# Performance work log

Measured on AMD Instinct MI355X. Metric: run time of the kernel, lower is better.

The kernel has to match this reference:

```python
import jax, jax.numpy as jnp
import numpy as np

AB = 8            # activation quant bits
NOISE_LEVEL = 0.1
CY_SCALE = 2.0    # stands in for args.cy_scale
B, IN, H = 8192, 512, 512


def _fake_quant(x, bits, sign):
    # forward: clip/clamp then round-to-grid; backward (STE) handled elsewhere
    if sign:
        delta = 1.0 / (2.0 ** (bits - 1))
        xc = jnp.clip(x, -1.0 + delta, 1.0 - delta)
        scale = 2.0 ** (bits - 1)
    else:
        xc = jnp.clip(x, 0.0, 1.0)
        scale = 2.0 ** bits
    q = jnp.round(xc * scale) / scale
    # STE: identity gradient w.r.t. x
    return x + jax.lax.stop_gradient(q - x)


def setup_inputs() -> dict:
    key = jax.random.key(0)
    ks = jax.random.split(key, 11)
    return {
        "input": jax.random.normal(ks[0], (B, IN), jnp.float32),
        "hx": jax.random.normal(ks[1], (B, H), jnp.float32),
        "cx": jax.random.normal(ks[2], (B, H), jnp.float32),
        "weight_ih": jax.random.normal(ks[3], (4 * H, IN), jnp.float32),
        "weight_hh": jax.random.normal(ks[4], (4 * H, H), jnp.float32),
        "bias_ih": jax.random.normal(ks[5], (4 * H,), jnp.float32),
        "bias_hh": jax.random.normal(ks[6], (4 * H,), jnp.float32),
        "noise_ih": jax.random.normal(ks[7], (IN, 4 * H), jnp.float32),
        "noise_hh": jax.random.normal(ks[8], (H, 4 * H), jnp.float32),
        "noise_bias_ih": jax.random.normal(ks[9], (4 * H,), jnp.float32),
        "noise_bias_hh": jax.random.normal(ks[10], (4 * H,), jnp.float32),
    }


def reference(input, hx, cx, weight_ih, weight_hh, bias_ih, bias_hh,
              noise_ih, noise_hh, noise_bias_ih, noise_bias_hh):
    # noisy weights: noise = randn * w.max() * noise_level (raw randn passed in)
    w_ih = weight_ih.T + noise_ih * (jnp.max(weight_ih) * NOISE_LEVEL)   # [IN,4H]
    w_hh = weight_hh.T + noise_hh * (jnp.max(weight_hh) * NOISE_LEVEL)   # [H,4H]
    b_ih = bias_ih + noise_bias_ih * (jnp.max(bias_ih) * NOISE_LEVEL)
    b_hh = bias_hh + noise_bias_hh * (jnp.max(bias_hh) * NOISE_LEVEL)

    gates = input @ w_ih + b_ih + hx @ w_hh + b_hh                        # [B,4H]
    ingate, forgetgate, cellgate, outgate = jnp.split(gates, 4, axis=1)

    ingate = _fake_quant(jax.nn.sigmoid(ingate), AB, False)
    forgetgate = _fake_quant(jax.nn.sigmoid(forgetgate), AB, False)
    cellgate = _fake_quant(jnp.tanh(cellgate), AB, True)
    outgate = _fake_quant(jax.nn.sigmoid(outgate), AB, False)

    cy = _fake_quant(
        (_fake_quant(forgetgate * cx, AB, True)
         + _fake_quant(ingate * cellgate, AB, True)) / CY_SCALE,
        AB, True)
    hy = _fake_quant(
        outgate * _fake_quant(jnp.tanh(cy * CY_SCALE), AB, True),
        AB, True)
    return (hy, cy)
```

## Files before the change

### kernel.cpp

```cpp
#include <hip/hip_runtime.h>
#include <cstdint>

typedef unsigned short u16;
typedef __bf16 bf16x8 __attribute__((ext_vector_type(8)));
typedef float f32x4 __attribute__((ext_vector_type(4)));

#define NB 8192
#define HD 512
#define KD 1024
#define ND 2048
#define HY_OFF (NB * HD)
#define NT 32

__device__ __forceinline__ u16 f2bf(float f) {
  unsigned u = __float_as_uint(f);
  u += 0x7FFFu + ((u >> 16) & 1u);
  return (u16)(u >> 16);
}
__device__ __forceinline__ float bf2f(u16 h) {
  return __uint_as_float(((unsigned)h) << 16);
}
__device__ __forceinline__ void atomicMaxF(float* a, float v) {
  if (v >= 0.f) atomicMax((int*)a, __float_as_int(v));
  else          atomicMin((unsigned int*)a, __float_as_uint(v));
}
__device__ __forceinline__ float fq_u(float x) {
  float xc = fminf(fmaxf(x, 0.0f), 1.0f);
  return rintf(xc * 256.0f) * (1.0f / 256.0f);
}
__device__ __forceinline__ float fq_s(float x) {
  const float lim = 1.0f - 1.0f / 128.0f;
  float xc = fminf(fmaxf(x, -lim), lim);
  return rintf(xc * 128.0f) * (1.0f / 128.0f);
}
__device__ __forceinline__ float sigm(float x) { return 1.0f / (1.0f + expf(-x)); }

__device__ __forceinline__ void gload_lds16(const u16* g, u16* l) {
  __builtin_amdgcn_global_load_lds(
      (const __attribute__((address_space(1))) void*)g,
      (__attribute__((address_space(3))) void*)l, 16, 0, 0);
}

__global__ __launch_bounds__(256) void k_prep_max(
    const float* __restrict__ w_ih, const float* __restrict__ w_hh,
    const float* __restrict__ b_ih, const float* __restrict__ b_hh,
    float* __restrict__ maxes) {
  int bid = blockIdx.x;
  const float* src; int slot, base;
  if (bid < 1024)      { src = w_ih; slot = 0; base = bid * 1024; }
  else if (bid < 2048) { src = w_hh; slot = 1; base = (bid - 1024) * 1024; }
  else if (bid < 2050) { src = b_ih; slot = 2; base = (bid - 2048) * 1024; }
  else                 { src = b_hh; slot = 3; base = (bid - 2050) * 1024; }
  float m = -INFINITY;
  for (int i = threadIdx.x; i < 1024; i += 256) m = fmaxf(m, src[base + i]);
  for (int k = 1; k < 64; k <<= 1) m = fmaxf(m, __shfl_xor(m, k, 64));
  __shared__ float sm[4];
  if ((threadIdx.x & 63) == 0) sm[threadIdx.x >> 6] = m;
  __syncthreads();
  if (threadIdx.x == 0) {
    m = fmaxf(fmaxf(sm[0], sm[1]), fmaxf(sm[2], sm[3]));
    atomicMaxF(&maxes[slot], m);
  }
}

__global__ __launch_bounds__(256) void k_prep_build(
    const float* __restrict__ input, const float* __restrict__ hx,
    const float* __restrict__ w_ih, const float* __restrict__ w_hh,
    const float* __restrict__ n_ih, const float* __restrict__ n_hh,
    const float* __restrict__ b_ih, const float* __restrict__ b_hh,
    const float* __restrict__ nb_ih, const float* __restrict__ nb_hh,
    const float* __restrict__ maxes,
    u16* __restrict__ Xhi, u16* __restrict__ Xlo,
    u16* __restrict__ Whi, u16* __restrict__ Wlo,
    float* __restrict__ biasC) {
  const int bid = blockIdx.x;
  if (bid < 2048) {
    const int total4 = NB * KD / 4;
    for (int e4 = bid * 256 + threadIdx.x; e4 < total4; e4 += 2048 * 256) {
      int row = e4 >> 8;
      int c4  = e4 & 255;
      float4 v = (c4 < 128)
          ? reinterpret_cast<const float4*>(input)[row * 128 + c4]
          : reinterpret_cast<const float4*>(hx)[row * 128 + (c4 - 128)];
      float xs[4] = {v.x, v.y, v.z, v.w};
      ushort4 hi, lo;
      u16 h0 = f2bf(xs[0]); u16 l0 = f2bf(xs[0] - bf2f(h0));
      u16 h1 = f2bf(xs[1]); u16 l1 = f2bf(xs[1] - bf2f(h1));
      u16 h2 = f2bf(xs[2]); u16 l2 = f2bf(xs[2] - bf2f(h2));
      u16 h3 = f2bf(xs[3]); u16 l3 = f2bf(xs[3] - bf2f(h3));
      hi.x = h0; hi.y = h1; hi.z = h2; hi.w = h3;
      lo.x = l0; lo.y = l1; lo.z = l2; lo.w = l3;
      reinterpret_cast<ushort4*>(Xhi)[e4] = hi;
      reinterpret_cast<ushort4*>(Xlo)[e4] = lo;
    }
  } else if (bid < 2176) {
    __shared__ float nT[1024][17];
    const int w  = bid - 2048;
    const int j0 = w * 16;
    const int g  = ((j0 >> 7) & 1) * 2 + ((j0 >> 4) & 1);
    const int hb = ((j0 >> 8) << 2) | ((j0 >> 5) & 3);
    const int col0 = g * 512 + (hb << 4);
    {
      const int cl = threadIdx.x & 15;
      const int kr = threadIdx.x >> 4;
#pragma unroll 4
      for (int i = 0; i < 64; ++i) {
        const int k = kr + 16 * i;
        nT[k][cl] = (k < 512) ? n_ih[k * ND + col0 + cl]
                              : n_hh[(k - 512) * ND + col0 + cl];
      }
    }
    __syncthreads();
    const float s_ih = maxes[0] * 0.1f, s_hh = maxes[1] * 0.1f;
    const int c  = threadIdx.x >> 4;
    const int kl = threadIdx.x & 15;
    const int colL = col0 + c;
    const int j = j0 + c;
#pragma unroll 4
    for (int kk = 0; kk < 16; ++kk) {
      const int k = kk * 64 + kl * 4;
      float4 wv; float s;
      if (k < 512) {
        wv = reinterpret_cast<const float4*>(w_ih)[(colL * 512 + k) >> 2];
        s = s_ih;
      } else {
        wv = reinterpret_cast<const float4*>(w_hh)[(colL * 512 + k - 512) >> 2];
        s = s_hh;
      }
      float xs[4] = {wv.x + nT[k + 0][c] * s, wv.y + nT[k + 1][c] * s,
                     wv.z + nT[k + 2][c] * s, wv.w + nT[k + 3][c] * s};
      ushort4 hi, lo;
      u16 h0 = f2bf(xs[0]); u16 l0 = f2bf(xs[0] - bf2f(h0));
      u16 h1 = f2bf(xs[1]); u16 l1 = f2bf(xs[1] - bf2f(h1));
      u16 h2 = f2bf(xs[2]); u16 l2 = f2bf(xs[2] - bf2f(h2));
      u16 h3 = f2bf(xs[3]); u16 l3 = f2bf(xs[3] - bf2f(h3));
      hi.x = h0; hi.y = h1; hi.z = h2; hi.w = h3;
      lo.x = l0; lo.y = l1; lo.z = l2; lo.w = l3;
      reinterpret_cast<ushort4*>(Whi)[(j * KD + k) >> 2] = hi;
      reinterpret_cast<ushort4*>(Wlo)[(j * KD + k) >> 2] = lo;
    }
  } else {
    int j = (bid - 2176) * 256 + threadIdx.x;
    if (j < ND) {
      int g  = ((j >> 7) & 1) * 2 + ((j >> 4) & 1);
      int hb = ((j >> 8) << 2) | ((j >> 5) & 3);
      int col = g * 512 + (hb << 4) + (j & 15);
      biasC[j] = b_ih[col] + nb_ih[col] * (maxes[2] * 0.1f)
               + b_hh[col] + nb_hh[col] * (maxes[3] * 0.1f);
    }
  }
}

__global__ __launch_bounds__(512, 2) void k_gemm_lstm(
    const u16* __restrict__ Xhi, const u16* __restrict__ Xlo,
    const u16* __restrict__ Whi, const u16* __restrict__ Wlo,
    const float* __restrict__ biasC, const float* __restrict__ cx,
    float* __restrict__ out) {
  __shared__ u16 L[2][4][8192];
  const int tid  = threadIdx.x;
  const int lane = tid & 63, wid = tid >> 6;
  const int wr = wid >> 2, wc = wid & 3;
  const int lr = lane & 15, lg = lane >> 4;
  const int xcd = blockIdx.x & 7, tt = blockIdx.x >> 3;
  const int bm = ((xcd >> 1) << 3) | (tt & 7);
  const int bn = ((xcd & 1) << 2) | (tt >> 3);
  const int mbase = bm * 256, nbase = bn * 256;

  const int l8 = lane >> 3, l7 = lane & 7;
  const int csrc  = l7 ^ l8;
  const int srow  = wid * 16 + 2 * l8 + (csrc >> 2);
  const int skoff = (csrc & 3) * 8;
  const int sdst  = wid * 512;

  const int fro = (lr >> 1) * 64 + ((((lr & 1) << 2) | lg) ^ ((lr >> 1) & 7)) * 8;

  f32x4 acc[8][4] = {};
  bf16x8 afr[4][2];
  bf16x8 bfr[2][2][2];

#define STAGE(V, BUF, HALF)                                                   \
  {                                                                           \
    const u16* arr_ = (BUF) == 0 ? Xhi : (BUF) == 1 ? Xlo                     \
                      : (BUF) == 2 ? Whi : Wlo;                               \
    const int gb_ = ((BUF) < 2 ? mbase : nbase) + (HALF) * 128 + srow;        \
    gload_lds16(arr_ + (size_t)gb_ * KD + (V) * 32 + skoff,                   \
                &L[(V) & 1][(BUF)][(HALF) * 4096 + sdst]);                    \
  }

#define PH2(MH, STAGE_CODE, WAIT_CODE)                                       \
  {                                                                          \
    _Pragma("unroll") for (int m2 = 0; m2 < 4; ++m2) {                       \
      const int ab = ((MH) * 128 + wr * 64 + m2 * 16) * 32 + fro;            \
      afr[m2][0] = *reinterpret_cast<const bf16x8*>(&L[s][0][ab]);           \
      afr[m2][1] = *reinterpret_cast<const bf16x8*>(&L[s][1][ab]);           \
    }                                                                        \
    if ((MH) == 0) {                                                         \
      _Pragma("unroll") for (int nh = 0; nh < 2; ++nh)                       \
        _Pragma("unroll") for (int n2 = 0; n2 < 2; ++n2) {                   \
          const int bb = (nh * 128 + wc * 32 + n2 * 16) * 32 + fro;          \
          bfr[nh][n2][0] = *reinterpret_cast<const bf16x8*>(&L[s][2][bb]);   \
          bfr[nh][n2][1] = *reinterpret_cast<const bf16x8*>(&L[s][3][bb]);   \
        }                                                                    \
    }                                                                        \
    STAGE_CODE;                                                              \
    WAIT_CODE;                                                               \
    __builtin_amdgcn_s_barrier();                                            \
    __builtin_amdgcn_s_setprio(1);                                           \
    _Pragma("unroll") for (int t = 0; t < 3; ++t)                            \
      _Pragma("unroll") for (int m2 = 0; m2 < 4; ++m2)                       \
        _Pragma("unroll") for (int nh = 0; nh < 2; ++nh)                     \
          _Pragma("unroll") for (int n2 = 0; n2 < 2; ++n2) {                 \
            f32x4* ac = &acc[(MH) * 4 + m2][nh * 2 + n2];                    \
            *ac = __builtin_amdgcn_mfma_f32_16x16x32_bf16(                   \
                afr[m2][t == 1], bfr[nh][n2][t == 2], *ac, 0, 0, 0);         \
          }                                                                  \
    __builtin_amdgcn_s_setprio(0);                                           \
    __builtin_amdgcn_s_barrier();                                            \
  }

  STAGE(0, 0, 0); STAGE(0, 1, 0);
  STAGE(0, 2, 0); STAGE(0, 2, 1);
  STAGE(0, 3, 0); STAGE(0, 3, 1);
  STAGE(0, 0, 1); STAGE(0, 1, 1);
  asm volatile("s_waitcnt vmcnt(2)" ::: "memory");
  __builtin_amdgcn_s_barrier();

  int s = 0;
  for (int u = 0; u < NT - 1; ++u, s ^= 1) {
    PH2(0,
        { STAGE(u + 1, 0, 0); STAGE(u + 1, 1, 0);
          STAGE(u + 1, 2, 0); STAGE(u + 1, 2, 1);
          STAGE(u + 1, 3, 0); STAGE(u + 1, 3, 1); },
        asm volatile("s_waitcnt vmcnt(6)" ::: "memory"));
    PH2(1,
        { STAGE(u + 1, 0, 1); STAGE(u + 1, 1, 1); },
        asm volatile("s_waitcnt vmcnt(2)" ::: "memory"));
  }
  PH2(0, , asm volatile("s_waitcnt vmcnt(0)" ::: "memory"));
  PH2(1, , );

#undef PH2
#undef STAGE

  const int hb = bn * 4 + wc;
  const int h = hb * 16 + lr;
  float bias[4];
#pragma unroll
  for (int g = 0; g < 4; ++g)
    bias[g] = biasC[bn * 256 + ((g >> 1) * 8 + wc * 2 + (g & 1)) * 16 + lr];
#pragma unroll
  for (int mh = 0; mh < 2; ++mh) {
#pragma unroll
    for (int m2 = 0; m2 < 4; ++m2) {
      const int m = mh * 4 + m2;
#pragma unroll
      for (int r = 0; r < 4; ++r) {
        const int row = mbase + mh * 128 + wr * 64 + m2 * 16 + lg * 4 + r;
        const float gi = acc[m][0][r] + bias[0];
        const float gf = acc[m][1][r] + bias[1];
        const float gc = acc[m][2][r] + bias[2];
        const float go = acc[m][3][r] + bias[3];
        const float ig = fq_u(sigm(gi));
        const float fg = fq_u(sigm(gf));
        const float cg = fq_s(tanhf(gc));
        const float og = fq_u(sigm(go));
        const float cxv = cx[(size_t)row * HD + h];
        const float t1 = fq_s(fg * cxv);
        const float t2 = fq_s(ig * cg);
        const float cyv = fq_s((t1 + t2) * 0.5f);
        const float hyv = fq_s(og * fq_s(tanhf(cyv * 2.0f)));
        out[(size_t)row * HD + h] = hyv;
        out[HY_OFF + (size_t)row * HD + h] = cyv;
      }
    }
  }
}

extern "C" void kernel_launch(void* const* d_in, const int* in_sizes, int n_in,
                              void* d_out, int out_size, void* d_ws, size_t ws_size,
                              hipStream_t stream) {
  const float* input = (const float*)d_in[0];
  const float* hx    = (const float*)d_in[1];
  const float* cx    = (const float*)d_in[2];
  const float* w_ih  = (const float*)d_in[3];
  const float* w_hh  = (const float*)d_in[4];
  const float* b_ih  = (const float*)d_in[5];
  const float* b_hh  = (const float*)d_in[6];
  const float* n_ih  = (const float*)d_in[7];
  const float* n_hh  = (const float*)d_in[8];
  const float* nb_ih = (const float*)d_in[9];
  const float* nb_hh = (const float*)d_in[10];
  float* out = (float*)d_out;

  char* ws = (char*)d_ws;
  float* maxes = (float*)ws;
  u16* Xhi = (u16*)(ws + 256);
  u16* Xlo = (u16*)(ws + 256 + 16777216);
  u16* Whi = (u16*)(ws + 256 + 2 * 16777216);
  u16* Wlo = (u16*)(ws + 256 + 2 * 16777216 + 4194304);
  float* biasC = (float*)(ws + 256 + 2 * 16777216 + 2 * 4194304);

  hipMemsetAsync(maxes, 0xFF, 16, stream);
  hipLaunchKernelGGL(k_prep_max, dim3(2052), dim3(256), 0, stream,
                     w_ih, w_hh, b_ih, b_hh, maxes);
  hipLaunchKernelGGL(k_prep_build, dim3(2184), dim3(256), 0, stream,
                     input, hx, w_ih, w_hh, n_ih, n_hh, b_ih, b_hh,
                     nb_ih, nb_hh, maxes, Xhi, Xlo, Whi, Wlo, biasC);
  hipLaunchKernelGGL(k_gemm_lstm, dim3(256), dim3(512), 0, stream,
                     Xhi, Xlo, Whi, Wlo, biasC, cx, out);
}
```

Measured before the change: 150.8 us.

## Switch GEMM to 32x32x16 MFMA with quarter-phase pipeline and shuffle epilogue

Replaces the 16x16x32 bf16 MFMA tiling with 32x32x16 instructions, which need fewer LDS fragment loads per FLOP. The main loop is split into four quarter phases per K-tile with finer-grained staging and vmcnt waits, and is unrolled by two so the double-buffer slot is a compile-time constant. The epilogue uses cross-lane shuffles to pair the gate values, since the new accumulator layout gives each lane only two of the four gates, and half the lanes write hy while the other half write cy. The cost is more barriers per tile and more complicated index and swizzle logic, which could introduce bank conflicts or correctness errors.

```diff
diff --git a/kernel.cpp b/kernel.cpp
--- a/kernel.cpp
+++ b/kernel.cpp
@@ -3,7 +3,7 @@
 
 typedef unsigned short u16;
 typedef __bf16 bf16x8 __attribute__((ext_vector_type(8)));
-typedef float f32x4 __attribute__((ext_vector_type(4)));
+typedef float f32x16 __attribute__((ext_vector_type(16)));
 
 #define NB 8192
 #define HD 512
@@ -160,7 +160,6 @@
   const int tid  = threadIdx.x;
   const int lane = tid & 63, wid = tid >> 6;
   const int wr = wid >> 2, wc = wid & 3;
-  const int lr = lane & 15, lg = lane >> 4;
   const int xcd = blockIdx.x & 7, tt = blockIdx.x >> 3;
   const int bm = ((xcd >> 1) << 3) | (tt & 7);
   const int bn = ((xcd & 1) << 2) | (tt >> 3);
@@ -172,106 +171,122 @@
   const int skoff = (csrc & 3) * 8;
   const int sdst  = wid * 512;
 
-  const int fro = (lr >> 1) * 64 + ((((lr & 1) << 2) | lg) ^ ((lr >> 1) & 7)) * 8;
-
-  f32x4 acc[8][4] = {};
-  bf16x8 afr[4][2];
+  const int l31 = lane & 31, hi32 = lane >> 5;
+  const int lh  = l31 >> 1;
+  const int cb0 = (((lane & 1) << 2) | hi32) ^ (lh & 7);
+
+  f32x16 acc[4][2] = {};
+  bf16x8 afr[2][2][2];
   bf16x8 bfr[2][2][2];
 
-#define STAGE(V, BUF, HALF)                                                   \
+#define STAGE(V, SLOT, BUF, HALF)                                             \
   {                                                                           \
     const u16* arr_ = (BUF) == 0 ? Xhi : (BUF) == 1 ? Xlo                     \
                       : (BUF) == 2 ? Whi : Wlo;                               \
     const int gb_ = ((BUF) < 2 ? mbase : nbase) + (HALF) * 128 + srow;        \
     gload_lds16(arr_ + (size_t)gb_ * KD + (V) * 32 + skoff,                   \
-                &L[(V) & 1][(BUF)][(HALF) * 4096 + sdst]);                    \
-  }
-
-#define PH2(MH, STAGE_CODE, WAIT_CODE)                                       \
-  {                                                                          \
-    _Pragma("unroll") for (int m2 = 0; m2 < 4; ++m2) {                       \
-      const int ab = ((MH) * 128 + wr * 64 + m2 * 16) * 32 + fro;            \
-      afr[m2][0] = *reinterpret_cast<const bf16x8*>(&L[s][0][ab]);           \
-      afr[m2][1] = *reinterpret_cast<const bf16x8*>(&L[s][1][ab]);           \
-    }                                                                        \
-    if ((MH) == 0) {                                                         \
-      _Pragma("unroll") for (int nh = 0; nh < 2; ++nh)                       \
-        _Pragma("unroll") for (int n2 = 0; n2 < 2; ++n2) {                   \
-          const int bb = (nh * 128 + wc * 32 + n2 * 16) * 32 + fro;          \
-          bfr[nh][n2][0] = *reinterpret_cast<const bf16x8*>(&L[s][2][bb]);   \
-          bfr[nh][n2][1] = *reinterpret_cast<const bf16x8*>(&L[s][3][bb]);   \
-        }                                                                    \
-    }                                                                        \
-    STAGE_CODE;                                                              \
-    WAIT_CODE;                                                               \
-    __builtin_amdgcn_s_barrier();                                            \
-    __builtin_amdgcn_s_setprio(1);                                           \
-    _Pragma("unroll") for (int t = 0; t < 3; ++t)                            \
-      _Pragma("unroll") for (int m2 = 0; m2 < 4; ++m2)                       \
-        _Pragma("unroll") for (int nh = 0; nh < 2; ++nh)                     \
-          _Pragma("unroll") for (int n2 = 0; n2 < 2; ++n2) {                 \
-            f32x4* ac = &acc[(MH) * 4 + m2][nh * 2 + n2];                    \
-            *ac = __builtin_amdgcn_mfma_f32_16x16x32_bf16(                   \
-                afr[m2][t == 1], bfr[nh][n2][t == 2], *ac, 0, 0, 0);         \
-          }                                                                  \
-    __builtin_amdgcn_s_setprio(0);                                           \
-    __builtin_amdgcn_s_barrier();                                            \
-  }
-
-  STAGE(0, 0, 0); STAGE(0, 1, 0);
-  STAGE(0, 2, 0); STAGE(0, 2, 1);
-  STAGE(0, 3, 0); STAGE(0, 3, 1);
-  STAGE(0, 0, 1); STAGE(0, 1, 1);
-  asm volatile("s_waitcnt vmcnt(2)" ::: "memory");
+                &L[(SLOT)][(BUF)][(HALF) * 4096 + sdst]);                     \
+  }
+
+#define PH32(S, MH, NH, LOADA, LOADB, STAGE_CODE, WAIT_CODE)                  \
+  {                                                                           \
+    if (LOADA) {                                                              \
+      _Pragma("unroll") for (int m2 = 0; m2 < 2; ++m2)                        \
+        _Pragma("unroll") for (int ks = 0; ks < 2; ++ks) {                    \
+          const int ao = (MH) * 4096 + (wr * 32 + m2 * 16 + lh) * 64          \
+                         + (cb0 ^ (ks << 1)) * 8;                             \
+          afr[m2][ks][0] = *reinterpret_cast<const bf16x8*>(&L[S][0][ao]);    \
+          afr[m2][ks][1] = *reinterpret_cast<const bf16x8*>(&L[S][1][ao]);    \
+        }                                                                     \
+    }                                                                         \
+    if (LOADB) {                                                              \
+      _Pragma("unroll") for (int ks = 0; ks < 2; ++ks) {                      \
+        const int bo = (NH) * 4096 + (wc * 16 + lh) * 64                      \
+                       + (cb0 ^ (ks << 1)) * 8;                               \
+        bfr[(NH)][ks][0] = *reinterpret_cast<const bf16x8*>(&L[S][2][bo]);    \
+        bfr[(NH)][ks][1] = *reinterpret_cast<const bf16x8*>(&L[S][3][bo]);    \
+      }                                                                       \
+    }                                                                         \
+    STAGE_CODE;                                                               \
+    WAIT_CODE;                                                                \
+    __builtin_amdgcn_s_barrier();                                             \
+    __builtin_amdgcn_s_setprio(1);                                            \
+    _Pragma("unroll") for (int t = 0; t < 3; ++t)                             \
+      _Pragma("unroll") for (int ks = 0; ks < 2; ++ks)                        \
+        _Pragma("unroll") for (int m2 = 0; m2 < 2; ++m2) {                    \
+          f32x16* ac = &acc[(MH) * 2 + m2][NH];                               \
+          *ac = __builtin_amdgcn_mfma_f32_32x32x16_bf16(                      \
+              afr[m2][ks][t == 1], bfr[(NH)][ks][t == 2], *ac, 0, 0, 0);      \
+        }                                                                     \
+    __builtin_amdgcn_s_setprio(0);                                            \
+    __builtin_amdgcn_s_barrier();                                             \
+  }
+
+#define V4 asm volatile("s_waitcnt vmcnt(4)" ::: "memory")
+#define V2 asm volatile("s_waitcnt vmcnt(2)" ::: "memory")
+
+#define TILE(U, S)                                                            \
+  PH32(S, 0, 0, 1, 1,                                                         \
+       { STAGE((U) + 1, (S) ^ 1, 0, 0); STAGE((U) + 1, (S) ^ 1, 1, 0); }, V4) \
+  PH32(S, 0, 1, 0, 1,                                                         \
+       { STAGE((U) + 1, (S) ^ 1, 2, 0); STAGE((U) + 1, (S) ^ 1, 3, 0); }, V4) \
+  PH32(S, 1, 1, 1, 0,                                                         \
+       { STAGE((U) + 1, (S) ^ 1, 2, 1); STAGE((U) + 1, (S) ^ 1, 3, 1); }, )   \
+  PH32(S, 1, 0, 0, 0,                                                         \
+       { STAGE((U) + 1, (S) ^ 1, 0, 1); STAGE((U) + 1, (S) ^ 1, 1, 1); }, V2)
+
+  STAGE(0, 0, 0, 0); STAGE(0, 0, 1, 0);
+  STAGE(0, 0, 2, 0); STAGE(0, 0, 3, 0);
+  STAGE(0, 0, 2, 1); STAGE(0, 0, 3, 1);
+  STAGE(0, 0, 0, 1); STAGE(0, 0, 1, 1);
+  V2;
   __builtin_amdgcn_s_barrier();
 
-  int s = 0;
-  for (int u = 0; u < NT - 1; ++u, s ^= 1) {
-    PH2(0,
-        { STAGE(u + 1, 0, 0); STAGE(u + 1, 1, 0);
-          STAGE(u + 1, 2, 0); STAGE(u + 1, 2, 1);
-          STAGE(u + 1, 3, 0); STAGE(u + 1, 3, 1); },
-        asm volatile("s_waitcnt vmcnt(6)" ::: "memory"));
-    PH2(1,
-        { STAGE(u + 1, 0, 1); STAGE(u + 1, 1, 1); },
-        asm volatile("s_waitcnt vmcnt(2)" ::: "memory"));
-  }
-  PH2(0, , asm volatile("s_waitcnt vmcnt(0)" ::: "memory"));
-  PH2(1, , );
-
-#undef PH2
+  for (int u = 0; u < NT - 2; u += 2) {
+    TILE(u, 0)
+    TILE(u + 1, 1)
+  }
+  TILE(NT - 2, 0)
+  PH32(1, 0, 0, 1, 1, , )
+  PH32(1, 0, 1, 0, 1, , asm volatile("s_waitcnt vmcnt(0)" ::: "memory"))
+  PH32(1, 1, 1, 1, 0, , )
+  PH32(1, 1, 0, 0, 0, , )
+
+#undef TILE
+#undef V4
+#undef V2
+#undef PH32
 #undef STAGE
 
-  const int hb = bn * 4 + wc;
-  const int h = hb * 16 + lr;
-  float bias[4];
+  const int b = (lane >> 4) & 1;
+  const int h = (bn * 4 + wc) * 16 + (lane & 15);
+  const float bias0 = biasC[nbase + wc * 32 + l31];
+  const float bias1 = biasC[nbase + 128 + wc * 32 + l31];
 #pragma unroll
-  for (int g = 0; g < 4; ++g)
-    bias[g] = biasC[bn * 256 + ((g >> 1) * 8 + wc * 2 + (g & 1)) * 16 + lr];
+  for (int m = 0; m < 4; ++m) {
 #pragma unroll
-  for (int mh = 0; mh < 2; ++mh) {
-#pragma unroll
-    for (int m2 = 0; m2 < 4; ++m2) {
-      const int m = mh * 4 + m2;
-#pragma unroll
-      for (int r = 0; r < 4; ++r) {
-        const int row = mbase + mh * 128 + wr * 64 + m2 * 16 + lg * 4 + r;
-        const float gi = acc[m][0][r] + bias[0];
-        const float gf = acc[m][1][r] + bias[1];
-        const float gc = acc[m][2][r] + bias[2];
-        const float go = acc[m][3][r] + bias[3];
-        const float ig = fq_u(sigm(gi));
-        const float fg = fq_u(sigm(gf));
-        const float cg = fq_s(tanhf(gc));
-        const float og = fq_u(sigm(go));
-        const float cxv = cx[(size_t)row * HD + h];
-        const float t1 = fq_s(fg * cxv);
-        const float t2 = fq_s(ig * cg);
-        const float cyv = fq_s((t1 + t2) * 0.5f);
-        const float hyv = fq_s(og * fq_s(tanhf(cyv * 2.0f)));
-        out[(size_t)row * HD + h] = hyv;
-        out[HY_OFF + (size_t)row * HD + h] = cyv;
-      }
+    for (int r = 0; r < 16; ++r) {
+      const int row = mbase + (m >> 1) * 128 + wr * 64 + (m & 1) * 32
+                      + (r & 3) + 8 * (r >> 2) + 4 * hi32;
+      const float v0 = acc[m][0][r] + bias0;
+      const float v1 = acc[m][1][r] + bias1;
+      const float w0 = __shfl_xor(v0, 16, 64);
+      const float w1 = __shfl_xor(v1, 16, 64);
+      const float gi = b ? w0 : v0;
+      const float gf = b ? v0 : w0;
+      const float gc = b ? w1 : v1;
+      const float go = b ? v1 : w1;
+      const float ig = fq_u(sigm(gi));
+      const float fg = fq_u(sigm(gf));
+      const float cg = fq_s(tanhf(gc));
+      const float og = fq_u(sigm(go));
+      const float cxv = cx[(size_t)row * HD + h];
+      const float t1 = fq_s(fg * cxv);
+      const float t2 = fq_s(ig * cg);
+      const float cyv = fq_s((t1 + t2) * 0.5f);
+      const float hyv = fq_s(og * fq_s(tanhf(cyv * 2.0f)));
+      if (b) out[HY_OFF + (size_t)row * HD + h] = cyv;
+      else   out[(size_t)row * HD + h] = hyv;
     }
   }
 }
```

Result: slower. 199.3 us (+32.2%).
